# Kernel tuning notes

Hardware: AMD Instinct MI355X
Metric: run time of the kernel (lower is better)

## Reference

```python
import jax, jax.numpy as jnp
import numpy as np

N = 50000      # num nodes
E = 800000     # num edges per edge set (before self loops)
F_IN = 256     # encoding_size
F_EMB = 256    # embedding_size
PE = 98        # d2an positional features (beijing)
ALPHA1 = 0.5
ALPHA2 = 0.5


def _uniform_linear(key, out_f, in_f):
    # torch.nn.Linear default init: U(-1/sqrt(in_f), 1/sqrt(in_f))
    s = 1.0 / np.sqrt(in_f)
    return jax.random.uniform(key, (out_f, in_f), jnp.float32, -s, s)


def setup_inputs() -> dict:
    key = jax.random.key(0)
    ks = jax.random.split(key, 18)
    inp = {
        'x': jax.random.normal(ks[0], (N, F_IN), jnp.float32),
        'd2an': jax.random.normal(ks[1], (N, PE), jnp.float32),
        'edge_index_l0': jax.random.randint(ks[2], (2, E), 0, N, jnp.int32),
        'edge_attr_l0': jax.random.uniform(ks[3], (E,), jnp.float32),
        'edge_index_l1': jax.random.randint(ks[4], (2, E), 0, N, jnp.int32),
        'edge_attr_l1': jax.random.uniform(ks[5], (E,), jnp.float32),
        # nodeLin of conv1/conv2 (used only on firstLayer with usePE)
        'Wnode1': _uniform_linear(ks[6], F_IN, F_IN + PE),
        'Wnode2': _uniform_linear(ks[7], F_IN, F_IN + PE),
        # lin1/lin2 of each conv layer (bias-free linears)
        'W11': _uniform_linear(ks[8], F_EMB, F_IN),
        'W12': _uniform_linear(ks[9], F_EMB, F_IN),
        'W21': _uniform_linear(ks[10], F_EMB, F_IN),
        'W22': _uniform_linear(ks[11], F_EMB, F_IN),
        'W31': _uniform_linear(ks[12], F_EMB, F_EMB),
        'W32': _uniform_linear(ks[13], F_EMB, F_EMB),
        'W41': _uniform_linear(ks[14], F_EMB, F_EMB),
        'W42': _uniform_linear(ks[15], F_EMB, F_EMB),
    }
    return inp


def _pos_knn_gnn_layer(x, row, col, attr, d2an, Wnode, W1, W2, first):
    """PosKnnGNNLayer.forward with useSI=True, usePE=True (eval mode).

    message = deg_norm * (x_j @ W1.T) + edge_norm * (x_j @ W2.T), scatter-add to col.
    Linearity lets us aggregate (norm * x_j) first, then apply W1/W2 once per node.
    """
    n = x.shape[0]
    loop = jnp.arange(n, dtype=row.dtype)
    row = jnp.concatenate([row, loop])          # source j
    col = jnp.concatenate([col, loop])          # target i
    attr = jnp.concatenate([attr, jnp.ones((n,), attr.dtype)])  # self-loop weight 1.0

    if first:
        x = jnp.concatenate([x, d2an], axis=1) @ Wnode.T  # [n, F_IN]

    deg = jax.ops.segment_sum(jnp.ones_like(attr), col, num_segments=n)
    dinv = jnp.where(deg > 0, deg ** -0.5, 0.0)
    deg_norm = dinv[row] * dinv[col]            # [E']

    einv = jnp.where(attr > 0, attr ** -0.5, 0.0)
    edge_norm = jnp.minimum(einv, 1.0)          # clamp values > 1.0 to 1.0

    xj = x[row]                                  # gather [E', F]
    a1 = jax.ops.segment_sum(deg_norm[:, None] * xj, col, num_segments=n)
    a2 = jax.ops.segment_sum(edge_norm[:, None] * xj, col, num_segments=n)
    return a1 @ W1.T + a2 @ W2.T                 # [n, F_EMB]


def reference(x, d2an, edge_index_l0, edge_attr_l0, edge_index_l1, edge_attr_l1,
              Wnode1, Wnode2, W11, W12, W21, W22, W31, W32, W41, W42):
    r0, c0 = edge_index_l0[0], edge_index_l0[1]
    r1, c1 = edge_index_l1[0], edge_index_l1[1]

    x0 = jax.nn.relu(_pos_knn_gnn_layer(x, r0, c0, edge_attr_l0, d2an, Wnode1, W11, W12, True))
    x1 = jax.nn.relu(_pos_knn_gnn_layer(x, r1, c1, edge_attr_l1, d2an, Wnode2, W21, W22, True))
    h = ALPHA1 * x0 + ALPHA2 * x1               # dropout p=0.3 is identity in eval

    x0 = jax.nn.relu(_pos_knn_gnn_layer(h, r0, c0, edge_attr_l0, None, None, W31, W32, False))
    x1 = jax.nn.relu(_pos_knn_gnn_layer(h, r1, c1, edge_attr_l1, None, None, W41, W42, False))
    return ALPHA1 * x0 + ALPHA2 * x1
```

## Files before the change

kernel.cpp:

```cpp
#include <hip/hip_runtime.h>


using bf16x8  = __attribute__((ext_vector_type(8))) __bf16;
using floatx4 = __attribute__((ext_vector_type(4))) float;
using f32x2   = __attribute__((ext_vector_type(2))) float;

__device__ __forceinline__ unsigned short f2b(float f) {
    unsigned u = __float_as_uint(f);
    return (unsigned short)((u + 0x7FFFu + ((u >> 16) & 1u)) >> 16);
}
__device__ __forceinline__ unsigned short f2h(float f) {
    _Float16 h = (_Float16)f;
    return __builtin_bit_cast(unsigned short, h);
}
__device__ __forceinline__ float h2f(unsigned short u) {
    return (float)__builtin_bit_cast(_Float16, u);
}

__global__ void k_front(
    const int* __restrict__ col0, const int* __restrict__ col1, int E,
    int* __restrict__ cnt0, int* __restrict__ cnt1,
    const float* __restrict__ x, const float* __restrict__ pe,
    unsigned short* __restrict__ xc,
    const float* __restrict__ Wn1, const float* __restrict__ Wn2,
    const float* __restrict__ W11, const float* __restrict__ W12,
    const float* __restrict__ W21, const float* __restrict__ W22,
    const float* __restrict__ W31, const float* __restrict__ W32,
    const float* __restrict__ W41, const float* __restrict__ W42,
    unsigned short* __restrict__ wn0c, unsigned short* __restrict__ wn1c,
    unsigned short* __restrict__ wc0, unsigned short* __restrict__ wc1,
    unsigned short* __restrict__ wc2, unsigned short* __restrict__ wc3,
    int n, int F, int PEd, int KC, int KP) {
    int idx = blockIdx.x * 256 + threadIdx.x;
    if (idx < E) { atomicAdd(&cnt0[col0[idx]], 1); return; }
    idx -= E;
    if (idx < E) { atomicAdd(&cnt1[col1[idx]], 1); return; }
    idx -= E;
    const int CH = KP >> 3;
    const int NXC = n * CH;
    if (idx < NXC) {
        int i = idx / CH, c = idx - i * CH;
        int k = c << 3;
        uint4 o;
        if (k + 8 <= F) {
            const float4* px = (const float4*)(x + (size_t)i * F + k);
            float4 v0 = px[0];
            float4 v1 = px[1];
            o.x = (unsigned)f2b(v0.x) | ((unsigned)f2b(v0.y) << 16);
            o.y = (unsigned)f2b(v0.z) | ((unsigned)f2b(v0.w) << 16);
            o.z = (unsigned)f2b(v1.x) | ((unsigned)f2b(v1.y) << 16);
            o.w = (unsigned)f2b(v1.z) | ((unsigned)f2b(v1.w) << 16);
        } else if (k < KC) {
            const float* pp = pe + (size_t)i * PEd + (k - F);
            int rem = KC - k;
            float e0 = pp[0];
            float e1 = (1 < rem) ? pp[1] : 0.f;
            float e2 = (2 < rem) ? pp[2] : 0.f;
            float e3 = (3 < rem) ? pp[3] : 0.f;
            float e4 = (4 < rem) ? pp[4] : 0.f;
            float e5 = (5 < rem) ? pp[5] : 0.f;
            float e6 = (6 < rem) ? pp[6] : 0.f;
            float e7 = (7 < rem) ? pp[7] : 0.f;
            o.x = (unsigned)f2b(e0) | ((unsigned)f2b(e1) << 16);
            o.y = (unsigned)f2b(e2) | ((unsigned)f2b(e3) << 16);
            o.z = (unsigned)f2b(e4) | ((unsigned)f2b(e5) << 16);
            o.w = (unsigned)f2b(e6) | ((unsigned)f2b(e7) << 16);
        } else {
            o.x = o.y = o.z = o.w = 0u;
        }
        *(uint4*)(xc + (size_t)idx * 8) = o;
        return;
    }
    idx -= NXC;
    int npad = F * KP;
    if (idx < 2 * npad) {
        const float* W = (idx < npad) ? Wn1 : Wn2;
        unsigned short* Wc = (idx < npad) ? wn0c : wn1c;
        int t = (idx < npad) ? idx : idx - npad;
        int o = t / KP, k = t - o * KP;
        Wc[t] = f2b(k < KC ? W[(size_t)o * KC + k] : 0.0f);
        return;
    }
    int t = idx - 2 * npad;
    int seg = F * 512;
    if (t >= 4 * seg) return;
    int which = t / seg;
    int r = t - which * seg;
    const float* Wa = (which == 0) ? W11 : (which == 1) ? W21 : (which == 2) ? W31 : W41;
    const float* Wb = (which == 0) ? W12 : (which == 1) ? W22 : (which == 2) ? W32 : W42;
    unsigned short* Wc = (which == 0) ? wc0 : (which == 1) ? wc1 : (which == 2) ? wc2 : wc3;
    int o = r >> 9, k = r & 511;
    float v = (k < 256) ? Wa[(size_t)o * 256 + k] : Wb[(size_t)o * 256 + (k - 256)];
    Wc[r] = f2b(v);
}

__global__ __launch_bounds__(1024) void k_scanA(
    const int* __restrict__ cnt0, const int* __restrict__ cnt1,
    int* __restrict__ off0, int* __restrict__ off1,
    int* __restrict__ bs0, int* __restrict__ bs1, int n) {
    const int* cnt = blockIdx.y ? cnt1 : cnt0;
    int* off = blockIdx.y ? off1 : off0;
    int* bs  = blockIdx.y ? bs1 : bs0;
    __shared__ int wsum[16];
    __shared__ int wpre[16];
    const int t = threadIdx.x;
    const int lane = t & 63;
    const int w = t >> 6;
    const int i = blockIdx.x * 1024 + t;
    int v = (i < n) ? ((cnt[i] + 4) & ~3) : 0;
    #pragma unroll
    for (int d = 1; d < 64; d <<= 1) {
        int u = __shfl_up(v, d, 64);
        if (lane >= d) v += u;
    }
    if (lane == 63) wsum[w] = v;
    __syncthreads();
    if (t < 16) {
        int s2 = wsum[t];
        #pragma unroll
        for (int d = 1; d < 16; d <<= 1) {
            int u = __shfl_up(s2, d, 16);
            if (t >= d) s2 += u;
        }
        wpre[t] = s2;
    }
    __syncthreads();
    int incl = v + (w > 0 ? wpre[w - 1] : 0);
    if (i < n) off[i + 1] = incl;
    if (t == 1023) bs[blockIdx.x] = incl;
}

__global__ void k_scanB(int* __restrict__ bs0, int* __restrict__ bs1, int nb) {
    int* bs = blockIdx.y ? bs1 : bs0;
    const int t = threadIdx.x;
    int v = (t < nb) ? bs[t] : 0;
    int orig = v;
    #pragma unroll
    for (int d = 1; d < 64; d <<= 1) {
        int u = __shfl_up(v, d, 64);
        if (t >= d) v += u;
    }
    if (t < nb) bs[t] = v - orig;
}

__global__ __launch_bounds__(1024) void k_scanC(
    const int* __restrict__ bs0, const int* __restrict__ bs1,
    const int* __restrict__ cnt0, const int* __restrict__ cnt1,
    int* __restrict__ off0, int* __restrict__ off1,
    float* __restrict__ dinv0, float* __restrict__ dinv1,
    int* __restrict__ cur0, int* __restrict__ cur1, int n) {
    int* off = blockIdx.y ? off1 : off0;
    const int* bs = blockIdx.y ? bs1 : bs0;
    const int* cnt = blockIdx.y ? cnt1 : cnt0;
    float* dinv = blockIdx.y ? dinv1 : dinv0;
    int* cur = blockIdx.y ? cur1 : cur0;
    const int i = blockIdx.x * 1024 + threadIdx.x;
    if (i == 0) off[0] = 0;
    if (i < n) {
        int ci = cnt[i];
        int o = off[i + 1] + (blockIdx.x > 0 ? bs[blockIdx.x] : 0);
        off[i + 1] = o;
        cur[i] = o - ((ci + 4) & ~3);
        dinv[i] = rsqrtf((float)(ci + 1));
    }
}

__global__ void k_fillpad(
    const int* __restrict__ ei0, const float* __restrict__ ea0,
    const int* __restrict__ ei1, const float* __restrict__ ea1,
    int E, int EB,
    const int* __restrict__ cnt0, const int* __restrict__ cnt1,
    const int* __restrict__ off0, const int* __restrict__ off1,
    const float* __restrict__ dinv0, const float* __restrict__ dinv1,
    int* __restrict__ cur0, int* __restrict__ cur1,
    uint2* __restrict__ rec0, uint2* __restrict__ rec1, int n) {
    const int s = blockIdx.y;
    const float* dinv = s ? dinv1 : dinv0;
    uint2* rec = s ? rec1 : rec0;
    int t = blockIdx.x * 256 + threadIdx.x;
    if (t < EB) {
        int e = t;
        if (e >= E) return;
        const int* ei = s ? ei1 : ei0;
        const float* ea = s ? ea1 : ea0;
        int* cur = s ? cur1 : cur0;
        int r = ei[e];
        int c = ei[E + e];
        float a = ea[e];
        float w2 = (a > 0.0f) ? fminf(rsqrtf(a), 1.0f) : 0.0f;
        float w1 = dinv[r] * dinv[c];
        int p = atomicAdd(&cur[c], 1);
        rec[p] = make_uint2((unsigned)r,
                            ((unsigned)f2h(w1) << 16) | (unsigned)f2h(w2));
    } else {
        int i = t - EB;
        if (i >= n) return;
        const int* cnt = s ? cnt1 : cnt0;
        const int* off = s ? off1 : off0;
        int p = off[i] + cnt[i], pe = off[i + 1];
        float di = dinv[i];
        rec[p++] = make_uint2((unsigned)i,
                              ((unsigned)f2h(di * di) << 16) | 0x3C00u);
        for (; p < pe; ++p) rec[p] = make_uint2(0u, 0u);
    }
}


#define AGG4(g, wsel)                                                         \
    do {                                                                      \
        float w1 = h2f((unsigned short)((wsel) >> 16));                       \
        float w2 = h2f((unsigned short)((wsel) & 0xFFFFu));                   \
        f32x2 w1v = {w1, w1};                                                 \
        f32x2 w2v = {w2, w2};                                                 \
        f32x2 v;                                                              \
        v.x = __uint_as_float((g).x << 16);                                   \
        v.y = __uint_as_float((g).x & 0xFFFF0000u);                           \
        c1a = __builtin_elementwise_fma(w1v, v, c1a);                         \
        c2a = __builtin_elementwise_fma(w2v, v, c2a);                         \
        v.x = __uint_as_float((g).y << 16);                                   \
        v.y = __uint_as_float((g).y & 0xFFFF0000u);                           \
        c1b = __builtin_elementwise_fma(w1v, v, c1b);                         \
        c2b = __builtin_elementwise_fma(w2v, v, c2b);                         \
    } while (0)

__global__ __launch_bounds__(256) void k_agg(
    const unsigned short* __restrict__ X0, const unsigned short* __restrict__ X1,
    const int* __restrict__ off0, const int* __restrict__ off1,
    const uint2* __restrict__ rec0, const uint2* __restrict__ rec1,
    unsigned short* __restrict__ A0, unsigned short* __restrict__ A1, int n) {
    const int s = blockIdx.y;
    const unsigned short* X = s ? X1 : X0;
    const int* off = s ? off1 : off0;
    const uint2* rec = s ? rec1 : rec0;
    unsigned short* A = s ? A1 : A0;

    const int gw = (blockIdx.x * 256 + threadIdx.x) >> 6;
    const int lane = threadIdx.x & 63;
    if (gw >= n) return;

    const int e0 = __builtin_amdgcn_readfirstlane(off[gw]);
    const int e1 = __builtin_amdgcn_readfirstlane(off[gw + 1]);
    const uint2* X2 = (const uint2*)X;

    f32x2 c1a = {0.f, 0.f}, c1b = {0.f, 0.f};
    f32x2 c2a = {0.f, 0.f}, c2b = {0.f, 0.f};

    const uint4* recq = (const uint4*)(rec + e0);
    const int nit = (e1 - e0) >> 2;
    #pragma unroll 2
    for (int it = 0; it < nit; ++it) {
        uint4 qa = recq[it * 2];
        uint4 qb = recq[it * 2 + 1];
        unsigned s0 = (unsigned)__builtin_amdgcn_readfirstlane(qa.x);
        unsigned s1 = (unsigned)__builtin_amdgcn_readfirstlane(qa.z);
        unsigned s2 = (unsigned)__builtin_amdgcn_readfirstlane(qb.x);
        unsigned s3 = (unsigned)__builtin_amdgcn_readfirstlane(qb.z);
        uint2 g0 = X2[(size_t)s0 * 64 + lane];
        uint2 g1 = X2[(size_t)s1 * 64 + lane];
        uint2 g2 = X2[(size_t)s2 * 64 + lane];
        uint2 g3 = X2[(size_t)s3 * 64 + lane];
        AGG4(g0, qa.y);
        AGG4(g1, qa.w);
        AGG4(g2, qb.y);
        AGG4(g3, qb.w);
    }

    uint2 o1, o2;
    o1.x = (unsigned)f2b(c1a.x) | ((unsigned)f2b(c1a.y) << 16);
    o1.y = (unsigned)f2b(c1b.x) | ((unsigned)f2b(c1b.y) << 16);
    o2.x = (unsigned)f2b(c2a.x) | ((unsigned)f2b(c2a.y) << 16);
    o2.y = (unsigned)f2b(c2b.x) | ((unsigned)f2b(c2b.y) << 16);
    *(uint2*)(A + (size_t)gw * 512 + lane * 4) = o1;
    *(uint2*)(A + (size_t)gw * 512 + 256 + lane * 4) = o2;
}

#define GLL(g, l) \
    __builtin_amdgcn_global_load_lds((__attribute__((address_space(1))) void*)(g), \
                                     (__attribute__((address_space(3))) void*)(l), 16, 0, 0)

__global__ __launch_bounds__(256) void gemm_bt(
    const unsigned short* __restrict__ A,
    const unsigned short* __restrict__ B0, const unsigned short* __restrict__ B1,
    int M, int K, int Nc,
    unsigned short* __restrict__ outH0, unsigned short* __restrict__ outH1) {
    const unsigned short* B = blockIdx.z ? B1 : B0;
    unsigned short* outH = blockIdx.z ? outH1 : outH0;

    __shared__ __align__(16) unsigned short sA[128 * 32];
    __shared__ __align__(16) unsigned short sB[128 * 32];
    const int tid = threadIdx.x;
    const int lane = tid & 63;
    const int wave = tid >> 6;
    const int bm = blockIdx.x * 128;
    const int bn = blockIdx.y * 128;

    const int r0 = wave * 32 + (lane >> 2);
    const int kcol = (lane & 3) * 8;
    const int ga0 = min(bm + r0, M - 1);
    const int ga1 = min(bm + r0 + 16, M - 1);
    const int gb0 = min(bn + r0, Nc - 1);
    const int gb1 = min(bn + r0 + 16, Nc - 1);
    const unsigned short* pa0 = A + (size_t)ga0 * K + kcol;
    const unsigned short* pa1 = A + (size_t)ga1 * K + kcol;
    const unsigned short* pb0 = B + (size_t)gb0 * K + kcol;
    const unsigned short* pb1 = B + (size_t)gb1 * K + kcol;
    unsigned short* la0 = &sA[wave * 1024];
    unsigned short* la1 = &sA[wave * 1024 + 512];
    unsigned short* lb0 = &sB[wave * 1024];
    unsigned short* lb1 = &sB[wave * 1024 + 512];

    floatx4 acc[4][4];
    #pragma unroll
    for (int i = 0; i < 4; i++)
        #pragma unroll
        for (int j = 0; j < 4; j++) acc[i][j] = (floatx4){0.f, 0.f, 0.f, 0.f};

    const int mbase = (wave & 1) * 64 + (lane & 15);
    const int nbase = (wave >> 1) * 64 + (lane & 15);
    const int koff = (lane >> 4) * 8;

    for (int kk = 0; kk < K; kk += 32) {
        GLL(pa0 + kk, la0);
        GLL(pa1 + kk, la1);
        GLL(pb0 + kk, lb0);
        GLL(pb1 + kk, lb1);
        __syncthreads();
        bf16x8 af[4], bf[4];
        #pragma unroll
        for (int mi = 0; mi < 4; mi++)
            af[mi] = *(const bf16x8*)&sA[(mbase + mi * 16) * 32 + koff];
        #pragma unroll
        for (int ni = 0; ni < 4; ni++)
            bf[ni] = *(const bf16x8*)&sB[(nbase + ni * 16) * 32 + koff];
        #pragma unroll
        for (int mi = 0; mi < 4; mi++)
            #pragma unroll
            for (int ni = 0; ni < 4; ni++)
                acc[mi][ni] = __builtin_amdgcn_mfma_f32_16x16x32_bf16(
                    af[mi], bf[ni], acc[mi][ni], 0, 0, 0);
        __syncthreads();
    }

    const int crow = bm + (wave & 1) * 64 + (lane >> 4) * 4;
    const int ccol = bn + (wave >> 1) * 64 + (lane & 15);
    #pragma unroll
    for (int mi = 0; mi < 4; mi++)
        #pragma unroll
        for (int ni = 0; ni < 4; ni++)
            #pragma unroll
            for (int r = 0; r < 4; r++) {
                int row = crow + mi * 16 + r;
                if (row >= M) continue;
                int col = ccol + ni * 16;
                outH[(size_t)row * Nc + col] = f2b(acc[mi][ni][r]);
            }
}

__global__ __launch_bounds__(256) void gemm_dual(
    const unsigned short* __restrict__ A0, const unsigned short* __restrict__ B0,
    const unsigned short* __restrict__ A1, const unsigned short* __restrict__ B1,
    int M, int K, int Nc,
    float* __restrict__ outF, unsigned short* __restrict__ outH, float alpha) {
    __shared__ __align__(16) unsigned short sA[128 * 32];
    __shared__ __align__(16) unsigned short sB[128 * 32];
    const int tid = threadIdx.x;
    const int lane = tid & 63;
    const int wave = tid >> 6;
    const int bm = blockIdx.x * 128;
    const int bn = blockIdx.y * 128;

    const int r0 = wave * 32 + (lane >> 2);
    const int kcol = (lane & 3) * 8;
    const int ga0 = min(bm + r0, M - 1);
    const int ga1 = min(bm + r0 + 16, M - 1);
    const int gb0 = min(bn + r0, Nc - 1);
    const int gb1 = min(bn + r0 + 16, Nc - 1);
    unsigned short* la0 = &sA[wave * 1024];
    unsigned short* la1 = &sA[wave * 1024 + 512];
    unsigned short* lb0 = &sB[wave * 1024];
    unsigned short* lb1 = &sB[wave * 1024 + 512];

    const int mbase = (wave & 1) * 64 + (lane & 15);
    const int nbase = (wave >> 1) * 64 + (lane & 15);
    const int koff = (lane >> 4) * 8;

    floatx4 acc[4][4], res[4][4];

    #pragma unroll
    for (int pass = 0; pass < 2; pass++) {
        const unsigned short* A = pass ? A1 : A0;
        const unsigned short* B = pass ? B1 : B0;
        const unsigned short* pa0 = A + (size_t)ga0 * K + kcol;
        const unsigned short* pa1 = A + (size_t)ga1 * K + kcol;
        const unsigned short* pb0 = B + (size_t)gb0 * K + kcol;
        const unsigned short* pb1 = B + (size_t)gb1 * K + kcol;
        #pragma unroll
        for (int i = 0; i < 4; i++)
            #pragma unroll
            for (int j = 0; j < 4; j++) acc[i][j] = (floatx4){0.f, 0.f, 0.f, 0.f};

        for (int kk = 0; kk < K; kk += 32) {
            GLL(pa0 + kk, la0);
            GLL(pa1 + kk, la1);
            GLL(pb0 + kk, lb0);
            GLL(pb1 + kk, lb1);
            __syncthreads();
            bf16x8 af[4], bf[4];
            #pragma unroll
            for (int mi = 0; mi < 4; mi++)
                af[mi] = *(const bf16x8*)&sA[(mbase + mi * 16) * 32 + koff];
            #pragma unroll
            for (int ni = 0; ni < 4; ni++)
                bf[ni] = *(const bf16x8*)&sB[(nbase + ni * 16) * 32 + koff];
            #pragma unroll
            for (int mi = 0; mi < 4; mi++)
                #pragma unroll
                for (int ni = 0; ni < 4; ni++)
                    acc[mi][ni] = __builtin_amdgcn_mfma_f32_16x16x32_bf16(
                        af[mi], bf[ni], acc[mi][ni], 0, 0, 0);
            __syncthreads();
        }
        if (pass == 0) {
            #pragma unroll
            for (int mi = 0; mi < 4; mi++)
                #pragma unroll
                for (int ni = 0; ni < 4; ni++)
                    #pragma unroll
                    for (int r = 0; r < 4; r++)
                        res[mi][ni][r] = fmaxf(acc[mi][ni][r], 0.0f);
        }
    }

    const int crow = bm + (wave & 1) * 64 + (lane >> 4) * 4;
    const int ccol = bn + (wave >> 1) * 64 + (lane & 15);
    #pragma unroll
    for (int mi = 0; mi < 4; mi++)
        #pragma unroll
        for (int ni = 0; ni < 4; ni++)
            #pragma unroll
            for (int r = 0; r < 4; r++) {
                int row = crow + mi * 16 + r;
                if (row >= M) continue;
                int col = ccol + ni * 16;
                float v = alpha * (res[mi][ni][r] + fmaxf(acc[mi][ni][r], 0.0f));
                size_t idx = (size_t)row * Nc + col;
                if (outF) outF[idx] = v;
                else      outH[idx] = f2b(v);
            }
}


extern "C" void kernel_launch(void* const* d_in, const int* in_sizes, int n_in,
                              void* d_out, int out_size, void* d_ws, size_t ws_size,
                              hipStream_t stream) {
    const int F = 256;
    const int N = in_sizes[0] / F;
    const int PEd = in_sizes[1] / N;
    const int E = in_sizes[2] / 2;
    const int KC = F + PEd;
    const int KP = (KC + 31) & ~31;

    const float* x   = (const float*)d_in[0];
    const float* pe  = (const float*)d_in[1];
    const int*   ei0 = (const int*)d_in[2];
    const float* ea0 = (const float*)d_in[3];
    const int*   ei1 = (const int*)d_in[4];
    const float* ea1 = (const float*)d_in[5];
    const float* Wn1 = (const float*)d_in[6];
    const float* Wn2 = (const float*)d_in[7];
    const float* W11 = (const float*)d_in[8];
    const float* W12 = (const float*)d_in[9];
    const float* W21 = (const float*)d_in[10];
    const float* W22 = (const float*)d_in[11];
    const float* W31 = (const float*)d_in[12];
    const float* W32 = (const float*)d_in[13];
    const float* W41 = (const float*)d_in[14];
    const float* W42 = (const float*)d_in[15];
    float* out = (float*)d_out;

    char* p = (char*)d_ws;
    auto alloc = [&](size_t b) -> char* {
        char* r = p;
        p += (b + 255) & ~(size_t)255;
        return r;
    };
    int*   cnt0  = (int*)alloc((size_t)N * 4);
    int*   cnt1  = (int*)alloc((size_t)N * 4);
    int*   off0  = (int*)alloc((size_t)(N + 1) * 4);
    int*   off1  = (int*)alloc((size_t)(N + 1) * 4);
    int*   cur0  = (int*)alloc((size_t)N * 4);
    int*   cur1  = (int*)alloc((size_t)N * 4);
    float* dinv0 = (float*)alloc((size_t)N * 4);
    float* dinv1 = (float*)alloc((size_t)N * 4);
    int*   bs0   = (int*)alloc(64 * 4);
    int*   bs1   = (int*)alloc(64 * 4);
    uint2* rec0  = (uint2*)alloc(((size_t)E + 4ull * N) * 8);
    uint2* rec1  = (uint2*)alloc(((size_t)E + 4ull * N) * 8);
    unsigned short* wn0c = (unsigned short*)alloc((size_t)F * KP * 2);
    unsigned short* wn1c = (unsigned short*)alloc((size_t)F * KP * 2);
    unsigned short* wc0  = (unsigned short*)alloc((size_t)F * 512 * 2);
    unsigned short* wc1  = (unsigned short*)alloc((size_t)F * 512 * 2);
    unsigned short* wc2  = (unsigned short*)alloc((size_t)F * 512 * 2);
    unsigned short* wc3  = (unsigned short*)alloc((size_t)F * 512 * 2);
    unsigned short* xa   = (unsigned short*)alloc((size_t)N * 512 * 2);
    unsigned short* xb   = xa + (size_t)N * 256;
    unsigned short* h    = (unsigned short*)alloc((size_t)N * F * 2);
    unsigned short* a12  = (unsigned short*)alloc((size_t)N * 512 * 2);
    unsigned short* xc   = a12;
    unsigned short* a12bL1 = (unsigned short*)d_out;
    unsigned short* a12bL2 = xa;

    const int B = 256;
    const int gE = (E + B - 1) / B;
    const int gN = (N + B - 1) / B;
    const int gW = (N + 3) / 4;
    const int nb = (N + 1023) / 1024;
    dim3 gemm_grid((N + 127) / 128, 2);
    dim3 gemm_grid2((N + 127) / 128, 2, 2);

    hipMemsetAsync(cnt0, 0, (size_t)((char*)cur0 - (char*)cnt0) - 
                   ((size_t)(N + 1) * 4 + 255 & ~(size_t)255) * 0, stream);
    hipMemsetAsync(cnt0, 0, (size_t)((char*)off0 - (char*)cnt0), stream);
    {
        const int NXC = N * (KP >> 3);
        const int TOTW = 2 * F * KP + 4 * F * 512;
        long long tot = 2ll * E + NXC + TOTW;
        k_front<<<(unsigned)((tot + B - 1) / B), B, 0, stream>>>(
            ei0 + E, ei1 + E, E, cnt0, cnt1, x, pe, xc,
            Wn1, Wn2, W11, W12, W21, W22, W31, W32, W41, W42,
            wn0c, wn1c, wc0, wc1, wc2, wc3, N, F, PEd, KC, KP);
    }

    k_scanA<<<dim3(nb, 2), 1024, 0, stream>>>(cnt0, cnt1, off0, off1, bs0, bs1, N);
    k_scanB<<<dim3(1, 2), 64, 0, stream>>>(bs0, bs1, nb);
    k_scanC<<<dim3(nb, 2), 1024, 0, stream>>>(bs0, bs1, cnt0, cnt1, off0, off1,
                                              dinv0, dinv1, cur0, cur1, N);
    k_fillpad<<<dim3(gE + gN, 2), B, 0, stream>>>(
        ei0, ea0, ei1, ea1, E, gE * B, cnt0, cnt1, off0, off1,
        dinv0, dinv1, cur0, cur1, rec0, rec1, N);

    gemm_bt<<<gemm_grid2, B, 0, stream>>>(xc, wn0c, wn1c, N, KP, F, xa, xb);

    k_agg<<<dim3(gW, 2), B, 0, stream>>>(xa, xb, off0, off1, rec0, rec1,
                                         a12, a12bL1, N);
    gemm_dual<<<gemm_grid, B, 0, stream>>>(a12, wc0, a12bL1, wc1, N, 512, F,
                                           nullptr, h, 0.5f);

    k_agg<<<dim3(gW, 2), B, 0, stream>>>(h, h, off0, off1, rec0, rec1,
                                         a12, a12bL2, N);
    gemm_dual<<<gemm_grid, B, 0, stream>>>(a12, wc2, a12bL2, wc3, N, 512, F,
                                           out, nullptr, 0.5f);
}
```

Before: 707.9 us.

## Replace three-kernel prefix scan with atomic segment allocation and swap GEMM grid axes

The three scan kernels (block scan, block-sum scan, fixup) are replaced by one kernel in which each node reserves its padded CSR segment through an atomicAdd on a per-edge-set counter. Segment ends are now recomputed from cnt instead of off[i+1], so k_fillpad and k_agg also read the count array. Segments are no longer in node order, which can reduce locality of record reads in aggregation. The GEMM grids also put the N-column tiles on blockIdx.x, so adjacent blocks share the same A row tile, which may improve L2 reuse.

```diff
diff --git a/kernel.cpp b/kernel.cpp
--- a/kernel.cpp
+++ b/kernel.cpp
@@ -94,75 +94,24 @@
     Wc[r] = f2b(v);
 }
 
-__global__ __launch_bounds__(1024) void k_scanA(
+__global__ void k_alloc(
     const int* __restrict__ cnt0, const int* __restrict__ cnt1,
-    int* __restrict__ off0, int* __restrict__ off1,
-    int* __restrict__ bs0, int* __restrict__ bs1, int n) {
-    const int* cnt = blockIdx.y ? cnt1 : cnt0;
-    int* off = blockIdx.y ? off1 : off0;
-    int* bs  = blockIdx.y ? bs1 : bs0;
-    __shared__ int wsum[16];
-    __shared__ int wpre[16];
-    const int t = threadIdx.x;
-    const int lane = t & 63;
-    const int w = t >> 6;
-    const int i = blockIdx.x * 1024 + t;
-    int v = (i < n) ? ((cnt[i] + 4) & ~3) : 0;
-    #pragma unroll
-    for (int d = 1; d < 64; d <<= 1) {
-        int u = __shfl_up(v, d, 64);
-        if (lane >= d) v += u;
-    }
-    if (lane == 63) wsum[w] = v;
-    __syncthreads();
-    if (t < 16) {
-        int s2 = wsum[t];
-        #pragma unroll
-        for (int d = 1; d < 16; d <<= 1) {
-            int u = __shfl_up(s2, d, 16);
-            if (t >= d) s2 += u;
-        }
-        wpre[t] = s2;
-    }
-    __syncthreads();
-    int incl = v + (w > 0 ? wpre[w - 1] : 0);
-    if (i < n) off[i + 1] = incl;
-    if (t == 1023) bs[blockIdx.x] = incl;
-}
-
-__global__ void k_scanB(int* __restrict__ bs0, int* __restrict__ bs1, int nb) {
-    int* bs = blockIdx.y ? bs1 : bs0;
-    const int t = threadIdx.x;
-    int v = (t < nb) ? bs[t] : 0;
-    int orig = v;
-    #pragma unroll
-    for (int d = 1; d < 64; d <<= 1) {
-        int u = __shfl_up(v, d, 64);
-        if (t >= d) v += u;
-    }
-    if (t < nb) bs[t] = v - orig;
-}
-
-__global__ __launch_bounds__(1024) void k_scanC(
-    const int* __restrict__ bs0, const int* __restrict__ bs1,
-    const int* __restrict__ cnt0, const int* __restrict__ cnt1,
+    int* __restrict__ tot,
     int* __restrict__ off0, int* __restrict__ off1,
     float* __restrict__ dinv0, float* __restrict__ dinv1,
     int* __restrict__ cur0, int* __restrict__ cur1, int n) {
+    int i = blockIdx.x * 256 + threadIdx.x;
+    if (i >= n) return;
+    const int* cnt = blockIdx.y ? cnt1 : cnt0;
     int* off = blockIdx.y ? off1 : off0;
-    const int* bs = blockIdx.y ? bs1 : bs0;
-    const int* cnt = blockIdx.y ? cnt1 : cnt0;
     float* dinv = blockIdx.y ? dinv1 : dinv0;
     int* cur = blockIdx.y ? cur1 : cur0;
-    const int i = blockIdx.x * 1024 + threadIdx.x;
-    if (i == 0) off[0] = 0;
-    if (i < n) {
-        int ci = cnt[i];
-        int o = off[i + 1] + (blockIdx.x > 0 ? bs[blockIdx.x] : 0);
-        off[i + 1] = o;
-        cur[i] = o - ((ci + 4) & ~3);
-        dinv[i] = rsqrtf((float)(ci + 1));
-    }
+    int ci = cnt[i];
+    int pad = (ci + 4) & ~3;
+    int o = atomicAdd(&tot[blockIdx.y], pad);
+    off[i] = o;
+    cur[i] = o;
+    dinv[i] = rsqrtf((float)(ci + 1));
 }
 
 __global__ void k_fillpad(
@@ -197,7 +146,8 @@
         if (i >= n) return;
         const int* cnt = s ? cnt1 : cnt0;
         const int* off = s ? off1 : off0;
-        int p = off[i] + cnt[i], pe = off[i + 1];
+        int ci = cnt[i];
+        int p = off[i] + ci, pe = off[i] + ((ci + 4) & ~3);
         float di = dinv[i];
         rec[p++] = make_uint2((unsigned)i,
                               ((unsigned)f2h(di * di) << 16) | 0x3C00u);
@@ -225,11 +175,13 @@
 
 __global__ __launch_bounds__(256) void k_agg(
     const unsigned short* __restrict__ X0, const unsigned short* __restrict__ X1,
+    const int* __restrict__ cnt0, const int* __restrict__ cnt1,
     const int* __restrict__ off0, const int* __restrict__ off1,
     const uint2* __restrict__ rec0, const uint2* __restrict__ rec1,
     unsigned short* __restrict__ A0, unsigned short* __restrict__ A1, int n) {
     const int s = blockIdx.y;
     const unsigned short* X = s ? X1 : X0;
+    const int* cnt = s ? cnt1 : cnt0;
     const int* off = s ? off1 : off0;
     const uint2* rec = s ? rec1 : rec0;
     unsigned short* A = s ? A1 : A0;
@@ -239,14 +191,14 @@
     if (gw >= n) return;
 
     const int e0 = __builtin_amdgcn_readfirstlane(off[gw]);
-    const int e1 = __builtin_amdgcn_readfirstlane(off[gw + 1]);
+    const int cv = __builtin_amdgcn_readfirstlane(cnt[gw]);
     const uint2* X2 = (const uint2*)X;
 
     f32x2 c1a = {0.f, 0.f}, c1b = {0.f, 0.f};
     f32x2 c2a = {0.f, 0.f}, c2b = {0.f, 0.f};
 
     const uint4* recq = (const uint4*)(rec + e0);
-    const int nit = (e1 - e0) >> 2;
+    const int nit = ((cv + 4) & ~3) >> 2;
     #pragma unroll 2
     for (int it = 0; it < nit; ++it) {
         uint4 qa = recq[it * 2];
@@ -283,16 +235,16 @@
     const unsigned short* __restrict__ B0, const unsigned short* __restrict__ B1,
     int M, int K, int Nc,
     unsigned short* __restrict__ outH0, unsigned short* __restrict__ outH1) {
-    const unsigned short* B = blockIdx.z ? B1 : B0;
-    unsigned short* outH = blockIdx.z ? outH1 : outH0;
+    const unsigned short* B = blockIdx.y ? B1 : B0;
+    unsigned short* outH = blockIdx.y ? outH1 : outH0;
 
     __shared__ __align__(16) unsigned short sA[128 * 32];
     __shared__ __align__(16) unsigned short sB[128 * 32];
     const int tid = threadIdx.x;
     const int lane = tid & 63;
     const int wave = tid >> 6;
-    const int bm = blockIdx.x * 128;
-    const int bn = blockIdx.y * 128;
+    const int bm = blockIdx.z * 128;
+    const int bn = blockIdx.x * 128;
 
     const int r0 = wave * 32 + (lane >> 2);
     const int kcol = (lane & 3) * 8;
@@ -366,8 +318,8 @@
     const int tid = threadIdx.x;
     const int lane = tid & 63;
     const int wave = tid >> 6;
-    const int bm = blockIdx.x * 128;
-    const int bn = blockIdx.y * 128;
+    const int bm = blockIdx.y * 128;
+    const int bn = blockIdx.x * 128;
 
     const int r0 = wave * 32 + (lane >> 2);
     const int kcol = (lane & 3) * 8;
@@ -486,14 +438,13 @@
     };
     int*   cnt0  = (int*)alloc((size_t)N * 4);
     int*   cnt1  = (int*)alloc((size_t)N * 4);
-    int*   off0  = (int*)alloc((size_t)(N + 1) * 4);
-    int*   off1  = (int*)alloc((size_t)(N + 1) * 4);
+    int*   tot   = (int*)alloc(2 * 4);
+    int*   off0  = (int*)alloc((size_t)N * 4);
+    int*   off1  = (int*)alloc((size_t)N * 4);
     int*   cur0  = (int*)alloc((size_t)N * 4);
     int*   cur1  = (int*)alloc((size_t)N * 4);
     float* dinv0 = (float*)alloc((size_t)N * 4);
     float* dinv1 = (float*)alloc((size_t)N * 4);
-    int*   bs0   = (int*)alloc(64 * 4);
-    int*   bs1   = (int*)alloc(64 * 4);
     uint2* rec0  = (uint2*)alloc(((size_t)E + 4ull * N) * 8);
     uint2* rec1  = (uint2*)alloc(((size_t)E + 4ull * N) * 8);
     unsigned short* wn0c = (unsigned short*)alloc((size_t)F * KP * 2);
@@ -514,40 +465,36 @@
     const int gE = (E + B - 1) / B;
     const int gN = (N + B - 1) / B;
     const int gW = (N + 3) / 4;
-    const int nb = (N + 1023) / 1024;
-    dim3 gemm_grid((N + 127) / 128, 2);
-    dim3 gemm_grid2((N + 127) / 128, 2, 2);
-
-    hipMemsetAsync(cnt0, 0, (size_t)((char*)cur0 - (char*)cnt0) - 
-                   ((size_t)(N + 1) * 4 + 255 & ~(size_t)255) * 0, stream);
+    const int Mb = (N + 127) / 128;
+    dim3 dual_grid(2, Mb);
+    dim3 bt_grid(2, 2, Mb);
+
     hipMemsetAsync(cnt0, 0, (size_t)((char*)off0 - (char*)cnt0), stream);
     {
         const int NXC = N * (KP >> 3);
         const int TOTW = 2 * F * KP + 4 * F * 512;
-        long long tot = 2ll * E + NXC + TOTW;
-        k_front<<<(unsigned)((tot + B - 1) / B), B, 0, stream>>>(
+        long long totThreads = 2ll * E + NXC + TOTW;
+        k_front<<<(unsigned)((totThreads + B - 1) / B), B, 0, stream>>>(
             ei0 + E, ei1 + E, E, cnt0, cnt1, x, pe, xc,
             Wn1, Wn2, W11, W12, W21, W22, W31, W32, W41, W42,
             wn0c, wn1c, wc0, wc1, wc2, wc3, N, F, PEd, KC, KP);
     }
 
-    k_scanA<<<dim3(nb, 2), 1024, 0, stream>>>(cnt0, cnt1, off0, off1, bs0, bs1, N);
-    k_scanB<<<dim3(1, 2), 64, 0, stream>>>(bs0, bs1, nb);
-    k_scanC<<<dim3(nb, 2), 1024, 0, stream>>>(bs0, bs1, cnt0, cnt1, off0, off1,
-                                              dinv0, dinv1, cur0, cur1, N);
+    k_alloc<<<dim3(gN, 2), B, 0, stream>>>(cnt0, cnt1, tot, off0, off1,
+                                           dinv0, dinv1, cur0, cur1, N);
     k_fillpad<<<dim3(gE + gN, 2), B, 0, stream>>>(
         ei0, ea0, ei1, ea1, E, gE * B, cnt0, cnt1, off0, off1,
         dinv0, dinv1, cur0, cur1, rec0, rec1, N);
 
-    gemm_bt<<<gemm_grid2, B, 0, stream>>>(xc, wn0c, wn1c, N, KP, F, xa, xb);
-
-    k_agg<<<dim3(gW, 2), B, 0, stream>>>(xa, xb, off0, off1, rec0, rec1,
-                                         a12, a12bL1, N);
-    gemm_dual<<<gemm_grid, B, 0, stream>>>(a12, wc0, a12bL1, wc1, N, 512, F,
+    gemm_bt<<<bt_grid, B, 0, stream>>>(xc, wn0c, wn1c, N, KP, F, xa, xb);
+
+    k_agg<<<dim3(gW, 2), B, 0, stream>>>(xa, xb, cnt0, cnt1, off0, off1,
+                                         rec0, rec1, a12, a12bL1, N);
+    gemm_dual<<<dual_grid, B, 0, stream>>>(a12, wc0, a12bL1, wc1, N, 512, F,
                                            nullptr, h, 0.5f);
 
-    k_agg<<<dim3(gW, 2), B, 0, stream>>>(h, h, off0, off1, rec0, rec1,
-                                         a12, a12bL2, N);
-    gemm_dual<<<gemm_grid, B, 0, stream>>>(a12, wc2, a12bL2, wc3, N, 512, F,
+    k_agg<<<dim3(gW, 2), B, 0, stream>>>(h, h, cnt0, cnt1, off0, off1,
+                                         rec0, rec1, a12, a12bL2, N);
+    gemm_dual<<<dual_grid, B, 0, stream>>>(a12, wc2, a12bL2, wc3, N, 512, F,
                                            out, nullptr, 0.5f);
 }
```

New measurement: 719.8 us. Within noise of the previous version (+1.7%).
